# Performance work log

Measured on AMD Instinct MI355X. Metric: run time of the kernel, lower is better.

The kernel has to match this reference:

```python
import jax, jax.numpy as jnp
import numpy as np

DIM = 768
NUM_HEADS = 12
HEAD_DIM = DIM // NUM_HEADS
HIDDEN = int(DIM * 4.0)
EPS = 1e-8


def layer_norm(x, w, b):
    mu = jnp.mean(x, axis=-1, keepdims=True)
    var = jnp.mean(jnp.square(x - mu), axis=-1, keepdims=True)
    return (x - mu) * jax.lax.rsqrt(var + EPS) * w + b


def setup_inputs() -> dict:
    key = jax.random.key(0)
    ks = jax.random.split(key, 10)
    s = 0.02
    return {
        "x": jax.random.normal(ks[0], (16, 4096, DIM), dtype=jnp.float32),
        # Linear weights stored as [in, out]
        "qkv_w": jax.random.normal(ks[1], (DIM, 3 * DIM), dtype=jnp.float32) * s,
        "qkv_b": jnp.zeros((3 * DIM,), dtype=jnp.float32),
        "proj_w": jax.random.normal(ks[2], (DIM, DIM), dtype=jnp.float32) * s,
        "proj_b": jnp.zeros((DIM,), dtype=jnp.float32),
        "fc1_w": jax.random.normal(ks[3], (DIM, HIDDEN), dtype=jnp.float32) * s,
        "fc1_b": jnp.zeros((HIDDEN,), dtype=jnp.float32),
        "fc2_w": jax.random.normal(ks[4], (HIDDEN, DIM), dtype=jnp.float32) * s,
        "fc2_b": jnp.zeros((DIM,), dtype=jnp.float32),
        "ln1_w": jnp.ones((DIM,), dtype=jnp.float32),
        "ln1_b": jnp.zeros((DIM,), dtype=jnp.float32),
        "ln2_w": jnp.ones((DIM,), dtype=jnp.float32),
        "ln2_b": jnp.zeros((DIM,), dtype=jnp.float32),
    }


def linear_attention(x, qkv_w, qkv_b, proj_w, proj_b):
    B, N, C = x.shape
    qkv = (x @ qkv_w + qkv_b).reshape(B, N, 3, NUM_HEADS, HEAD_DIM)
    qkv = qkv.transpose(2, 0, 3, 1, 4)  # [3, B, H, N, D]
    q, k, v = qkv[0], qkv[1], qkv[2]
    q = jax.nn.elu(q) + 1.0
    k = jax.nn.elu(k) + 1.0
    kv = jnp.einsum('bhsd,bhse->bhde', k, v)          # [B,H,D,D]
    z = 1.0 / jnp.einsum('bhsd,bhd->bhs', q, k.sum(axis=-2))  # [B,H,N]
    out = jnp.einsum('bhde,bhsd,bhs->bhse', kv, q, z)  # [B,H,N,D]
    out = out.transpose(0, 2, 1, 3).reshape(B, N, C)
    return out @ proj_w + proj_b


def reference(x, qkv_w, qkv_b, proj_w, proj_b, fc1_w, fc1_b, fc2_w, fc2_b,
              ln1_w, ln1_b, ln2_w, ln2_b):
    y = linear_attention(layer_norm(x, ln1_w, ln1_b), qkv_w, qkv_b, proj_w, proj_b)
    x = x + y
    h = layer_norm(x, ln2_w, ln2_b)
    h = jax.nn.gelu(h @ fc1_w + fc1_b, approximate=False) @ fc2_w + fc2_b
    return x + h
```

## Files before the change

### kernel.cpp

```cpp
#include <hip/hip_runtime.h>

#define DEVI __device__ __forceinline__

typedef __attribute__((ext_vector_type(8))) short bf16x8;
typedef __attribute__((ext_vector_type(4))) float f32x4;
typedef __attribute__((ext_vector_type(4))) unsigned short usx4;

DEVI float bf2f(unsigned short u) {
  unsigned int b = ((unsigned int)u) << 16;
  float f;
  __builtin_memcpy(&f, &b, 4);
  return f;
}
DEVI unsigned short f2bf(float f) {
  unsigned int x;
  __builtin_memcpy(&x, &f, 4);
  x += 0x7FFFu + ((x >> 16) & 1u);
  return (unsigned short)(x >> 16);
}
DEVI void gload_lds16(const void* g, void* l) {
  __builtin_amdgcn_global_load_lds((const __attribute__((address_space(1))) void*)g,
                                   (__attribute__((address_space(3))) void*)l,
                                   16, 0, 0);
}

__global__ __launch_bounds__(256) void wt_kernel(const float* __restrict__ W,
                                                 unsigned short* __restrict__ Wt,
                                                 int K, int N) {
  __shared__ float t[32][33];
  const int tx = threadIdx.x & 31, ty = threadIdx.x >> 5;
  const int n0 = blockIdx.x * 32, k0 = blockIdx.y * 32;
#pragma unroll
  for (int i = 0; i < 4; ++i)
    t[ty * 4 + i][tx] = W[(size_t)(k0 + ty * 4 + i) * N + n0 + tx];
  __syncthreads();
#pragma unroll
  for (int i = 0; i < 4; ++i)
    Wt[(size_t)(n0 + ty * 4 + i) * K + k0 + tx] = f2bf(t[tx][ty * 4 + i]);
}

__global__ __launch_bounds__(256) void ln_kernel(const float* __restrict__ x,
                                                 const float* __restrict__ w,
                                                 const float* __restrict__ b,
                                                 unsigned short* __restrict__ o) {
  const int lane = threadIdx.x & 63;
  const int wave = threadIdx.x >> 6;
  const size_t row = (size_t)blockIdx.x * 4 + wave;
  const float* xr = x + row * 768;
  float v[12];
  float s = 0.f, sq = 0.f;
#pragma unroll
  for (int i = 0; i < 3; ++i) {
    const float4 f = *(const float4*)&xr[i * 256 + lane * 4];
    v[i * 4 + 0] = f.x; v[i * 4 + 1] = f.y; v[i * 4 + 2] = f.z; v[i * 4 + 3] = f.w;
    s += f.x + f.y + f.z + f.w;
    sq += f.x * f.x + f.y * f.y + f.z * f.z + f.w * f.w;
  }
#pragma unroll
  for (int off = 32; off > 0; off >>= 1) {
    s += __shfl_xor(s, off);
    sq += __shfl_xor(sq, off);
  }
  const float mu = s * (1.f / 768.f);
  const float rs = rsqrtf(sq * (1.f / 768.f) - mu * mu + 1e-8f);
  unsigned short* orow = o + row * 768;
#pragma unroll
  for (int i = 0; i < 3; ++i) {
    usx4 st;
#pragma unroll
    for (int j = 0; j < 4; ++j) {
      const int c = i * 256 + lane * 4 + j;
      st[j] = f2bf((v[i * 4 + j] - mu) * rs * w[c] + b[c]);
    }
    *(usx4*)&orow[i * 256 + lane * 4] = st;
  }
}

__global__ __launch_bounds__(256) void fuse_kernel(const float* __restrict__ x,
                                                   const unsigned short* __restrict__ y,
                                                   const float* __restrict__ w,
                                                   const float* __restrict__ b,
                                                   float* __restrict__ x2,
                                                   unsigned short* __restrict__ o) {
  const int lane = threadIdx.x & 63;
  const int wave = threadIdx.x >> 6;
  const size_t row = (size_t)blockIdx.x * 4 + wave;
  const float* xr = x + row * 768;
  const unsigned short* yr = y + row * 768;
  float* x2r = x2 + row * 768;
  float v[12];
  float s = 0.f, sq = 0.f;
#pragma unroll
  for (int i = 0; i < 3; ++i) {
    const float4 f = *(const float4*)&xr[i * 256 + lane * 4];
    const usx4 yv = *(const usx4*)&yr[i * 256 + lane * 4];
    float t0 = f.x + bf2f(yv[0]);
    float t1 = f.y + bf2f(yv[1]);
    float t2 = f.z + bf2f(yv[2]);
    float t3 = f.w + bf2f(yv[3]);
    v[i * 4 + 0] = t0; v[i * 4 + 1] = t1; v[i * 4 + 2] = t2; v[i * 4 + 3] = t3;
    s += t0 + t1 + t2 + t3;
    sq += t0 * t0 + t1 * t1 + t2 * t2 + t3 * t3;
    float4 fo; fo.x = t0; fo.y = t1; fo.z = t2; fo.w = t3;
    *(float4*)&x2r[i * 256 + lane * 4] = fo;
  }
#pragma unroll
  for (int off = 32; off > 0; off >>= 1) {
    s += __shfl_xor(s, off);
    sq += __shfl_xor(sq, off);
  }
  const float mu = s * (1.f / 768.f);
  const float rs = rsqrtf(sq * (1.f / 768.f) - mu * mu + 1e-8f);
  unsigned short* orow = o + row * 768;
#pragma unroll
  for (int i = 0; i < 3; ++i) {
    usx4 st;
#pragma unroll
    for (int j = 0; j < 4; ++j) {
      const int c = i * 256 + lane * 4 + j;
      st[j] = f2bf((v[i * 4 + j] - mu) * rs * w[c] + b[c]);
    }
    *(usx4*)&orow[i * 256 + lane * 4] = st;
  }
}

template <int EPI>
__global__ __launch_bounds__(512, 2) void gemm256_k(
    const unsigned short* __restrict__ A, const unsigned short* __restrict__ Bt,
    const float* __restrict__ bias, int N, int K,
    unsigned short* __restrict__ O0, unsigned short* __restrict__ O1,
    unsigned short* __restrict__ O2, float* __restrict__ OF) {
  __shared__ char lds[131072];
  const int tid = threadIdx.x;
  const int lane = tid & 63, wave = tid >> 6;
  const int wr = wave >> 2, wc = wave & 3;

  const int gx = gridDim.x;
  const int nwg = gx * gridDim.y;
  const int cpx = nwg >> 3;
  const int wgid = blockIdx.x + gx * blockIdx.y;
  const int v = (wgid & 7) * cpx + (wgid >> 3);
  const size_t n0 = (size_t)(v % gx) * 256;
  const size_t m0 = (size_t)(v / gx) * 256;

  const size_t ldg = (size_t)K * 2;
  const char* Abase = (const char*)A + m0 * ldg;
  const char* Bbase = (const char*)Bt + n0 * ldg;

  const int q0 = tid, q1 = tid + 512;
  const int rp0 = q0 >> 3, rp1 = q1 >> 3;
  const int lc0 = (q0 & 7) ^ (rp0 & 7), lc1 = (q1 & 7) ^ (rp1 & 7);
  const size_t go0 = (size_t)(rp0 * 2 + (lc0 >> 2)) * ldg + (size_t)(lc0 & 3) * 16;
  const size_t go1 = (size_t)(rp1 * 2 + (lc1 >> 2)) * ldg + (size_t)(lc1 & 3) * 16;
  const char* aS0 = Abase + go0;
  const char* aS1 = Abase + go1;
  const char* bS0 = Bbase + go0;
  const char* bS1 = Bbase + go1;
  char* ldsb = (char*)lds;
  const int d0 = tid * 16, d1 = 8192 + tid * 16;

  f32x4 acc[8][4];
#pragma unroll
  for (int m = 0; m < 8; ++m)
#pragma unroll
    for (int n = 0; n < 4; ++n) acc[m][n] = f32x4{0.f, 0.f, 0.f, 0.f};

  const int L = lane & 15, kc4 = lane >> 4;
  const int pcv = (((L & 1) << 2) | kc4) ^ (L >> 1);
  const int aro = wr * 8192 + (L >> 1) * 128 + pcv * 16;
  const int bro = 16384 + wc * 4096 + (L >> 1) * 128 + pcv * 16;

  const int nt = K >> 5;

#define STAGE(tt)                                              \
  do {                                                         \
    char* dst_ = ldsb + ((tt) & 3) * 32768;                    \
    const size_t ko_ = (size_t)(tt) * 64;                      \
    gload_lds16(aS0 + ko_, dst_ + d0);                         \
    gload_lds16(aS1 + ko_, dst_ + d1);                         \
    gload_lds16(bS0 + ko_, dst_ + 16384 + d0);                 \
    gload_lds16(bS1 + ko_, dst_ + 16384 + d1);                 \
  } while (0)

  STAGE(0);
  STAGE(1);
  STAGE(2);

  for (int t = 0; t < nt; ++t) {
    const int rem = nt - t;
    if (rem > 2)
      asm volatile("s_waitcnt vmcnt(8) lgkmcnt(0)" ::: "memory");
    else if (rem == 2)
      asm volatile("s_waitcnt vmcnt(4) lgkmcnt(0)" ::: "memory");
    else
      asm volatile("s_waitcnt vmcnt(0) lgkmcnt(0)" ::: "memory");
    __builtin_amdgcn_s_barrier();
    asm volatile("" ::: "memory");
    if (t + 3 < nt) STAGE(t + 3);
    const char* base = ldsb + (t & 3) * 32768;
    bf16x8 bF[4];
#pragma unroll
    for (int n = 0; n < 4; ++n) bF[n] = *(const bf16x8*)(base + bro + n * 1024);
    {
      bf16x8 aF[4];
#pragma unroll
      for (int m = 0; m < 4; ++m) aF[m] = *(const bf16x8*)(base + aro + m * 1024);
      __builtin_amdgcn_s_setprio(1);
#pragma unroll
      for (int m = 0; m < 4; ++m)
#pragma unroll
        for (int n = 0; n < 4; ++n)
          acc[m][n] = __builtin_amdgcn_mfma_f32_16x16x32_bf16(aF[m], bF[n], acc[m][n], 0, 0, 0);
      __builtin_amdgcn_s_setprio(0);
    }
    {
      bf16x8 aF[4];
#pragma unroll
      for (int m = 0; m < 4; ++m) aF[m] = *(const bf16x8*)(base + aro + (m + 4) * 1024);
      __builtin_amdgcn_s_setprio(1);
#pragma unroll
      for (int m = 0; m < 4; ++m)
#pragma unroll
        for (int n = 0; n < 4; ++n)
          acc[m + 4][n] = __builtin_amdgcn_mfma_f32_16x16x32_bf16(aF[m], bF[n], acc[m + 4][n], 0, 0, 0);
      __builtin_amdgcn_s_setprio(0);
    }
  }
#undef STAGE

  const int rl = (lane >> 4) * 4;
  const int cl = lane & 15;
#pragma unroll
  for (int m = 0; m < 8; ++m) {
    const size_t r0 = m0 + wr * 128 + m * 16 + rl;
#pragma unroll
    for (int n = 0; n < 4; ++n) {
      const size_t c = n0 + wc * 64 + n * 16 + cl;
      const float bv = bias[c];
      if (EPI == 0) {
#pragma unroll
        for (int j = 0; j < 4; ++j) O0[(r0 + j) * (size_t)N + c] = f2bf(acc[m][n][j] + bv);
      } else if (EPI == 1) {
#pragma unroll
        for (int j = 0; j < 4; ++j) {
          float val = acc[m][n][j] + bv;
          val = 0.5f * val * (1.0f + erff(val * 0.70710678118654752f));
          O0[(r0 + j) * (size_t)N + c] = f2bf(val);
        }
      } else if (EPI == 2) {
        const int t = (int)(c / 768);
        const int rem = (int)c - t * 768;
        const int h = rem >> 6, d = rem & 63;
        const int b = (int)(r0 >> 12);
        const int s = (int)(r0 & 4095);
        const size_t bh = (size_t)b * 12 + h;
        if (t == 0) {
#pragma unroll
          for (int j = 0; j < 4; ++j) {
            float val = acc[m][n][j] + bv;
            val = val > 0.f ? val + 1.f : __expf(val);
            O0[(bh * 4096 + (size_t)(s + j)) * 64 + d] = f2bf(val);
          }
        } else {
          usx4 st;
#pragma unroll
          for (int j = 0; j < 4; ++j) {
            float val = acc[m][n][j] + bv;
            if (t == 1) val = val > 0.f ? val + 1.f : __expf(val);
            st[j] = f2bf(val);
          }
          unsigned short* dst = (t == 1) ? O1 : O2;
          *(usx4*)&dst[(bh * 64 + d) * 4096 + s] = st;
        }
      } else {
#pragma unroll
        for (int j = 0; j < 4; ++j) {
          const size_t idx = (r0 + j) * (size_t)N + c;
          OF[idx] += acc[m][n][j] + bv;
        }
      }
    }
  }
}

__global__ __launch_bounds__(256) void kv_kernel(const unsigned short* __restrict__ kT,
                                                 const unsigned short* __restrict__ vT,
                                                 float* __restrict__ kvT) {
  __shared__ float red[4 * 64 * 64];
  const int tid = threadIdx.x;
  const int lane = tid & 63, wave = tid >> 6;
  const size_t bh = blockIdx.x;
  const unsigned short* kb = kT + bh * (size_t)(64 * 4096);
  const unsigned short* vb = vT + bh * (size_t)(64 * 4096);
  f32x4 acc[4][4];
#pragma unroll
  for (int m = 0; m < 4; ++m)
#pragma unroll
    for (int n = 0; n < 4; ++n) acc[m][n] = f32x4{0.f, 0.f, 0.f, 0.f};
  const int kh = (lane >> 4) * 8;
  for (int st = 0; st < 32; ++st) {
    const int s0 = wave * 1024 + st * 32 + kh;
    bf16x8 aF[4], bF[4];
#pragma unroll
    for (int m = 0; m < 4; ++m)
      aF[m] = *(const bf16x8*)&kb[(size_t)((lane & 15) + 16 * m) * 4096 + s0];
#pragma unroll
    for (int n = 0; n < 4; ++n)
      bF[n] = *(const bf16x8*)&vb[(size_t)((lane & 15) + 16 * n) * 4096 + s0];
#pragma unroll
    for (int m = 0; m < 4; ++m)
#pragma unroll
      for (int n = 0; n < 4; ++n)
        acc[m][n] = __builtin_amdgcn_mfma_f32_16x16x32_bf16(aF[m], bF[n], acc[m][n], 0, 0, 0);
  }
#pragma unroll
  for (int m = 0; m < 4; ++m)
#pragma unroll
    for (int n = 0; n < 4; ++n)
#pragma unroll
      for (int j = 0; j < 4; ++j)
        red[wave * 4096 + (m * 16 + (lane >> 4) * 4 + j) * 64 + n * 16 + (lane & 15)] =
            acc[m][n][j];
  __syncthreads();
  for (int i = 0; i < 16; ++i) {
    const int f = i * 256 + tid;
    float s = 0.f;
#pragma unroll
    for (int w = 0; w < 4; ++w) s += red[w * 4096 + f];
    const int d = f >> 6, e = f & 63;
    kvT[bh * 4096 + e * 64 + d] = s;
  }
}

__global__ __launch_bounds__(256) void ksum_kernel(const unsigned short* __restrict__ kT,
                                                   float* __restrict__ ksum) {
  __shared__ float part[256];
  const int tid = threadIdx.x;
  const int d = tid & 63, p = tid >> 6;
  const size_t bh = blockIdx.x;
  const unsigned short* kb = kT + bh * (size_t)(64 * 4096) + (size_t)d * 4096 + p * 1024;
  float s = 0.f;
  for (int i = 0; i < 128; ++i) {
    const bf16x8 v = *(const bf16x8*)&kb[i * 8];
#pragma unroll
    for (int j = 0; j < 8; ++j) s += bf2f((unsigned short)v[j]);
  }
  part[tid] = s;
  __syncthreads();
  if (tid < 64) ksum[bh * 64 + d] = part[d] + part[64 + d] + part[128 + d] + part[192 + d];
}

__global__ __launch_bounds__(256) void attn_out_kernel(const unsigned short* __restrict__ q,
                                                       const float* __restrict__ kvT,
                                                       const float* __restrict__ ksum,
                                                       unsigned short* __restrict__ attnout) {
  __shared__ float kvl[4096];
  __shared__ float ksl[64];
  __shared__ float zl[4 * 64];
  const int tid = threadIdx.x;
  const int lane = tid & 63, wave = tid >> 6;
  const int bh = blockIdx.x >> 2;
  const int chunk = blockIdx.x & 3;
  const int b = bh / 12, h = bh % 12;
  const float* kvb = kvT + (size_t)bh * 4096;
  for (int i = tid; i < 4096; i += 256) kvl[i] = kvb[i];
  if (tid < 64) ksl[tid] = ksum[(size_t)bh * 64 + tid];
  __syncthreads();

  const int kh = (lane >> 4) * 8;
  bf16x8 bF[4], ksF;
#pragma unroll
  for (int n = 0; n < 4; ++n) {
    bf16x8 t;
#pragma unroll
    for (int j = 0; j < 8; ++j)
      t[j] = (short)f2bf(kvl[((lane & 15) + 16 * n) * 64 + kh + j]);
    bF[n] = t;
  }
  {
    bf16x8 t;
#pragma unroll
    for (int j = 0; j < 8; ++j)
      t[j] = ((lane & 15) == 0) ? (short)f2bf(ksl[kh + j]) : (short)0;
    ksF = t;
  }
  const unsigned short* qb = q + (size_t)bh * 4096 * 64;

  for (int st = 0; st < 4; ++st) {
    const int s0 = chunk * 1024 + wave * 256 + st * 64;
    bf16x8 aF[4];
#pragma unroll
    for (int m = 0; m < 4; ++m)
      aF[m] = *(const bf16x8*)&qb[(size_t)(s0 + (lane & 15) + 16 * m) * 64 + kh];
    f32x4 acc[4][4];
    f32x4 dacc[4];
#pragma unroll
    for (int m = 0; m < 4; ++m) {
      dacc[m] = f32x4{0.f, 0.f, 0.f, 0.f};
#pragma unroll
      for (int n = 0; n < 4; ++n) acc[m][n] = f32x4{0.f, 0.f, 0.f, 0.f};
    }
#pragma unroll
    for (int m = 0; m < 4; ++m) {
#pragma unroll
      for (int n = 0; n < 4; ++n)
        acc[m][n] = __builtin_amdgcn_mfma_f32_16x16x32_bf16(aF[m], bF[n], acc[m][n], 0, 0, 0);
      dacc[m] = __builtin_amdgcn_mfma_f32_16x16x32_bf16(aF[m], ksF, dacc[m], 0, 0, 0);
    }
    if ((lane & 15) == 0) {
#pragma unroll
      for (int m = 0; m < 4; ++m)
#pragma unroll
        for (int j = 0; j < 4; ++j)
          zl[wave * 64 + m * 16 + (lane >> 4) * 4 + j] = 1.0f / dacc[m][j];
    }
    __syncthreads();
#pragma unroll
    for (int m = 0; m < 4; ++m)
#pragma unroll
      for (int n = 0; n < 4; ++n)
#pragma unroll
        for (int j = 0; j < 4; ++j) {
          const int sl = m * 16 + (lane >> 4) * 4 + j;
          const int s = s0 + sl;
          const float val = acc[m][n][j] * zl[wave * 64 + sl];
          const int e = n * 16 + (lane & 15);
          attnout[((size_t)b * 4096 + s) * 768 + h * 64 + e] = f2bf(val);
        }
    __syncthreads();
  }
}

extern "C" void kernel_launch(void* const* d_in, const int* in_sizes, int n_in,
                              void* d_out, int out_size, void* d_ws, size_t ws_size,
                              hipStream_t stream) {
  const float* x = (const float*)d_in[0];
  const float* qkv_w = (const float*)d_in[1];
  const float* qkv_b = (const float*)d_in[2];
  const float* proj_w = (const float*)d_in[3];
  const float* proj_b = (const float*)d_in[4];
  const float* fc1_w = (const float*)d_in[5];
  const float* fc1_b = (const float*)d_in[6];
  const float* fc2_w = (const float*)d_in[7];
  const float* fc2_b = (const float*)d_in[8];
  const float* ln1_w = (const float*)d_in[9];
  const float* ln1_b = (const float*)d_in[10];
  const float* ln2_w = (const float*)d_in[11];
  const float* ln2_b = (const float*)d_in[12];
  float* out = (float*)d_out;

  char* ws = (char*)d_ws;
  const size_t PL = (size_t)65536 * 768 * 2;
  unsigned short* xn = (unsigned short*)(ws + 0 * PL);
  unsigned short* q = (unsigned short*)(ws + 1 * PL);
  unsigned short* kT = (unsigned short*)(ws + 2 * PL);
  unsigned short* vT = (unsigned short*)(ws + 3 * PL);
  unsigned short* attnout = xn;
  unsigned short* ybuf = kT;
  unsigned short* xn2 = (unsigned short*)(ws + 4 * PL);
  unsigned short* hbuf = (unsigned short*)(ws + 0 * PL);
  size_t off = 5 * PL;
  float* kvT = (float*)(ws + off); off += (size_t)192 * 4096 * 4;
  float* ksum = (float*)(ws + off); off += (size_t)192 * 64 * 4;
  unsigned short* qkvWt = (unsigned short*)(ws + off); off += (size_t)2304 * 768 * 2;
  unsigned short* projWt = (unsigned short*)(ws + off); off += (size_t)768 * 768 * 2;
  unsigned short* fc1Wt = (unsigned short*)(ws + off); off += (size_t)3072 * 768 * 2;
  unsigned short* fc2Wt = (unsigned short*)(ws + off); off += (size_t)768 * 3072 * 2;

  wt_kernel<<<dim3(72, 24), 256, 0, stream>>>(qkv_w, qkvWt, 768, 2304);
  wt_kernel<<<dim3(24, 24), 256, 0, stream>>>(proj_w, projWt, 768, 768);
  wt_kernel<<<dim3(96, 24), 256, 0, stream>>>(fc1_w, fc1Wt, 768, 3072);
  wt_kernel<<<dim3(24, 96), 256, 0, stream>>>(fc2_w, fc2Wt, 3072, 768);
  ln_kernel<<<16384, 256, 0, stream>>>(x, ln1_w, ln1_b, xn);
  gemm256_k<2><<<dim3(9, 256), 512, 0, stream>>>(xn, qkvWt, qkv_b, 2304, 768, q, kT, vT, nullptr);
  ksum_kernel<<<192, 256, 0, stream>>>(kT, ksum);
  kv_kernel<<<192, 256, 0, stream>>>(kT, vT, kvT);
  attn_out_kernel<<<768, 256, 0, stream>>>(q, kvT, ksum, attnout);
  gemm256_k<0><<<dim3(3, 256), 512, 0, stream>>>(attnout, projWt, proj_b, 768, 768, ybuf, nullptr,
                                                 nullptr, nullptr);
  fuse_kernel<<<16384, 256, 0, stream>>>(x, ybuf, ln2_w, ln2_b, out, xn2);
  gemm256_k<1><<<dim3(12, 256), 512, 0, stream>>>(xn2, fc1Wt, fc1_b, 3072, 768, hbuf, nullptr,
                                                  nullptr, nullptr);
  gemm256_k<3><<<dim3(3, 256), 512, 0, stream>>>(hbuf, fc2Wt, fc2_b, 768, 3072, nullptr, nullptr,
                                                 nullptr, out);
  (void)in_sizes; (void)n_in; (void)out_size; (void)ws_size;
}
```

Baseline: 1.734 ms.

## Split GEMM prefetch into A/B halves interleaved with MFMA and stage QKV transpose via LDS

The GEMM main loop now issues the A-tile prefetch and the B-tile prefetch separately, each placed between the two MFMA half-blocks with barriers and sched_barriers. This interleaves global-to-LDS traffic and LDS fragment reads with matrix math instead of issuing all loads at the top of the iteration. The QKV epilogue for the K and V transposed outputs is also rewritten to stage the tile in swizzled LDS per wave and then write contiguous rows along the sequence dimension. The wait-count logic is reworked to match, which risks subtle ordering errors and adds an extra barrier per iteration.

```diff
diff --git a/kernel.cpp b/kernel.cpp
--- a/kernel.cpp
+++ b/kernel.cpp
@@ -165,71 +165,136 @@
 #pragma unroll
     for (int n = 0; n < 4; ++n) acc[m][n] = f32x4{0.f, 0.f, 0.f, 0.f};
 
-  const int L = lane & 15, kc4 = lane >> 4;
+  const int L = lane & 15;
+  const int kc4 = lane >> 4;
   const int pcv = (((L & 1) << 2) | kc4) ^ (L >> 1);
   const int aro = wr * 8192 + (L >> 1) * 128 + pcv * 16;
   const int bro = 16384 + wc * 4096 + (L >> 1) * 128 + pcv * 16;
 
   const int nt = K >> 5;
 
-#define STAGE(tt)                                              \
+#define STAGE_A(tt)                                            \
   do {                                                         \
     char* dst_ = ldsb + ((tt) & 3) * 32768;                    \
     const size_t ko_ = (size_t)(tt) * 64;                      \
     gload_lds16(aS0 + ko_, dst_ + d0);                         \
     gload_lds16(aS1 + ko_, dst_ + d1);                         \
+  } while (0)
+#define STAGE_B(tt)                                            \
+  do {                                                         \
+    char* dst_ = ldsb + ((tt) & 3) * 32768;                    \
+    const size_t ko_ = (size_t)(tt) * 64;                      \
     gload_lds16(bS0 + ko_, dst_ + 16384 + d0);                 \
     gload_lds16(bS1 + ko_, dst_ + 16384 + d1);                 \
   } while (0)
 
-  STAGE(0);
-  STAGE(1);
-  STAGE(2);
+  STAGE_A(0); STAGE_B(0);
+  STAGE_A(1); STAGE_B(1);
+  STAGE_A(2); STAGE_B(2);
+  asm volatile("s_waitcnt vmcnt(8)" ::: "memory");
+  __builtin_amdgcn_s_barrier();
 
   for (int t = 0; t < nt; ++t) {
-    const int rem = nt - t;
-    if (rem > 2)
-      asm volatile("s_waitcnt vmcnt(8) lgkmcnt(0)" ::: "memory");
-    else if (rem == 2)
-      asm volatile("s_waitcnt vmcnt(4) lgkmcnt(0)" ::: "memory");
-    else
-      asm volatile("s_waitcnt vmcnt(0) lgkmcnt(0)" ::: "memory");
+    const char* base = ldsb + (t & 3) * 32768;
+    bf16x8 bF[4], aF0[4];
+#pragma unroll
+    for (int n = 0; n < 4; ++n) bF[n] = *(const bf16x8*)(base + bro + n * 1024);
+#pragma unroll
+    for (int m = 0; m < 4; ++m) aF0[m] = *(const bf16x8*)(base + aro + m * 1024);
+    if (t + 3 < nt) STAGE_A(t + 3);
+    asm volatile("s_waitcnt lgkmcnt(0)" ::: "memory");
     __builtin_amdgcn_s_barrier();
-    asm volatile("" ::: "memory");
-    if (t + 3 < nt) STAGE(t + 3);
-    const char* base = ldsb + (t & 3) * 32768;
-    bf16x8 bF[4];
-#pragma unroll
-    for (int n = 0; n < 4; ++n) bF[n] = *(const bf16x8*)(base + bro + n * 1024);
+    __builtin_amdgcn_sched_barrier(0);
+    __builtin_amdgcn_s_setprio(1);
+#pragma unroll
+    for (int m = 0; m < 4; ++m)
+#pragma unroll
+      for (int n = 0; n < 4; ++n)
+        acc[m][n] = __builtin_amdgcn_mfma_f32_16x16x32_bf16(aF0[m], bF[n], acc[m][n], 0, 0, 0);
+    __builtin_amdgcn_s_setprio(0);
+    __builtin_amdgcn_sched_barrier(0);
+    bf16x8 aF1[4];
+#pragma unroll
+    for (int m = 0; m < 4; ++m) aF1[m] = *(const bf16x8*)(base + aro + (m + 4) * 1024);
+    if (t + 3 < nt) STAGE_B(t + 3);
     {
-      bf16x8 aF[4];
-#pragma unroll
-      for (int m = 0; m < 4; ++m) aF[m] = *(const bf16x8*)(base + aro + m * 1024);
-      __builtin_amdgcn_s_setprio(1);
-#pragma unroll
-      for (int m = 0; m < 4; ++m)
-#pragma unroll
-        for (int n = 0; n < 4; ++n)
-          acc[m][n] = __builtin_amdgcn_mfma_f32_16x16x32_bf16(aF[m], bF[n], acc[m][n], 0, 0, 0);
-      __builtin_amdgcn_s_setprio(0);
-    }
-    {
-      bf16x8 aF[4];
-#pragma unroll
-      for (int m = 0; m < 4; ++m) aF[m] = *(const bf16x8*)(base + aro + (m + 4) * 1024);
-      __builtin_amdgcn_s_setprio(1);
-#pragma unroll
-      for (int m = 0; m < 4; ++m)
-#pragma unroll
-        for (int n = 0; n < 4; ++n)
-          acc[m + 4][n] = __builtin_amdgcn_mfma_f32_16x16x32_bf16(aF[m], bF[n], acc[m + 4][n], 0, 0, 0);
-      __builtin_amdgcn_s_setprio(0);
-    }
-  }
-#undef STAGE
+      const int rem = nt - t;
+      if (rem >= 4)
+        asm volatile("s_waitcnt vmcnt(8) lgkmcnt(0)" ::: "memory");
+      else if (rem == 3)
+        asm volatile("s_waitcnt vmcnt(4) lgkmcnt(0)" ::: "memory");
+      else
+        asm volatile("s_waitcnt vmcnt(0) lgkmcnt(0)" ::: "memory");
+    }
+    __builtin_amdgcn_s_barrier();
+    __builtin_amdgcn_sched_barrier(0);
+    __builtin_amdgcn_s_setprio(1);
+#pragma unroll
+    for (int m = 0; m < 4; ++m)
+#pragma unroll
+      for (int n = 0; n < 4; ++n)
+        acc[m + 4][n] = __builtin_amdgcn_mfma_f32_16x16x32_bf16(aF1[m], bF[n], acc[m + 4][n], 0, 0, 0);
+    __builtin_amdgcn_s_setprio(0);
+    __builtin_amdgcn_sched_barrier(0);
+  }
+#undef STAGE_A
+#undef STAGE_B
 
   const int rl = (lane >> 4) * 4;
   const int cl = lane & 15;
+
+  if (EPI == 2) {
+    const int cbase = (int)n0 + wc * 64;
+    const int tsec = cbase / 768;
+    const int h = (cbase - tsec * 768) >> 6;
+    const int rbase = (int)m0 + wr * 128;
+    const int b = rbase >> 12;
+    const int s0w = rbase & 4095;
+    const size_t bh = (size_t)b * 12 + h;
+    if (tsec == 0) {
+#pragma unroll
+      for (int m = 0; m < 8; ++m)
+#pragma unroll
+        for (int n = 0; n < 4; ++n) {
+          const int d = n * 16 + cl;
+          const float bv = bias[cbase + d];
+#pragma unroll
+          for (int j = 0; j < 4; ++j) {
+            float val = acc[m][n][j] + bv;
+            val = val > 0.f ? val + 1.f : __expf(val);
+            O0[(bh * 4096 + (size_t)(s0w + m * 16 + rl + j)) * 64 + d] = f2bf(val);
+          }
+        }
+    } else {
+      unsigned short* dst = (tsec == 1) ? O1 : O2;
+      char* wlds = ldsb + wave * 16384;
+#pragma unroll
+      for (int m = 0; m < 8; ++m)
+#pragma unroll
+        for (int n = 0; n < 4; ++n) {
+          const int c2 = n * 16 + cl;
+          const float bv = bias[cbase + c2];
+          usx4 st;
+#pragma unroll
+          for (int j = 0; j < 4; ++j) {
+            float val = acc[m][n][j] + bv;
+            if (tsec == 1) val = val > 0.f ? val + 1.f : __expf(val);
+            st[j] = f2bf(val);
+          }
+          const int r2 = m * 16 + rl;
+          *(usx4*)(wlds + c2 * 256 + ((r2 * 2) ^ ((c2 & 7) << 5))) = st;
+        }
+      asm volatile("s_waitcnt lgkmcnt(0)" ::: "memory");
+#pragma unroll 4
+      for (int dl = 0; dl < 64; ++dl) {
+        const unsigned int pr =
+            *(const unsigned int*)(wlds + dl * 256 + ((lane * 4) ^ ((dl & 7) << 5)));
+        *(unsigned int*)&dst[(bh * 64 + dl) * 4096 + (size_t)(s0w + lane * 2)] = pr;
+      }
+    }
+    return;
+  }
+
 #pragma unroll
   for (int m = 0; m < 8; ++m) {
     const size_t r0 = m0 + wr * 128 + m * 16 + rl;
@@ -246,31 +311,6 @@
           float val = acc[m][n][j] + bv;
           val = 0.5f * val * (1.0f + erff(val * 0.70710678118654752f));
           O0[(r0 + j) * (size_t)N + c] = f2bf(val);
-        }
-      } else if (EPI == 2) {
-        const int t = (int)(c / 768);
-        const int rem = (int)c - t * 768;
-        const int h = rem >> 6, d = rem & 63;
-        const int b = (int)(r0 >> 12);
-        const int s = (int)(r0 & 4095);
-        const size_t bh = (size_t)b * 12 + h;
-        if (t == 0) {
-#pragma unroll
-          for (int j = 0; j < 4; ++j) {
-            float val = acc[m][n][j] + bv;
-            val = val > 0.f ? val + 1.f : __expf(val);
-            O0[(bh * 4096 + (size_t)(s + j)) * 64 + d] = f2bf(val);
-          }
-        } else {
-          usx4 st;
-#pragma unroll
-          for (int j = 0; j < 4; ++j) {
-            float val = acc[m][n][j] + bv;
-            if (t == 1) val = val > 0.f ? val + 1.f : __expf(val);
-            st[j] = f2bf(val);
-          }
-          unsigned short* dst = (t == 1) ? O1 : O2;
-          *(usx4*)&dst[(bh * 64 + d) * 4096 + s] = st;
         }
       } else {
 #pragma unroll
```

New measurement: 1.637 ms. 5.6% less time.

## Shrink GEMM tiles to 128x256 with double buffering and fuse ksum into kv kernel

Applied to the files above, without the earlier changes.

The GEMM moves from a 256x256 tile with a 4-stage, 128KB LDS pipeline to a 128x256 tile with a 2-stage, 48KB LDS pipeline, aiming for higher occupancy and more workgroups. The QKV epilogue now writes K and V row-major ([bh, s, d]) instead of transposed, with per-wave head decoding. The kv kernel is rewritten to stage K and V chunks through swizzled LDS and to compute the k-sum in the same pass, dropping the separate ksum launch. The tradeoffs are lower per-tile data reuse, an extra barrier per K-step, and scalar strided epilogue stores.

```diff
diff --git a/kernel.cpp b/kernel.cpp
--- a/kernel.cpp
+++ b/kernel.cpp
@@ -125,12 +125,12 @@
 }
 
 template <int EPI>
-__global__ __launch_bounds__(512, 2) void gemm256_k(
+__global__ __launch_bounds__(512, 4) void gemm_k(
     const unsigned short* __restrict__ A, const unsigned short* __restrict__ Bt,
     const float* __restrict__ bias, int N, int K,
     unsigned short* __restrict__ O0, unsigned short* __restrict__ O1,
     unsigned short* __restrict__ O2, float* __restrict__ OF) {
-  __shared__ char lds[131072];
+  __shared__ unsigned short sm[24576];
   const int tid = threadIdx.x;
   const int lane = tid & 63, wave = tid >> 6;
   const int wr = wave >> 2, wc = wave & 3;
@@ -141,98 +141,99 @@
   const int wgid = blockIdx.x + gx * blockIdx.y;
   const int v = (wgid & 7) * cpx + (wgid >> 3);
   const size_t n0 = (size_t)(v % gx) * 256;
-  const size_t m0 = (size_t)(v / gx) * 256;
-
-  const size_t ldg = (size_t)K * 2;
-  const char* Abase = (const char*)A + m0 * ldg;
-  const char* Bbase = (const char*)Bt + n0 * ldg;
-
-  const int q0 = tid, q1 = tid + 512;
-  const int rp0 = q0 >> 3, rp1 = q1 >> 3;
-  const int lc0 = (q0 & 7) ^ (rp0 & 7), lc1 = (q1 & 7) ^ (rp1 & 7);
-  const size_t go0 = (size_t)(rp0 * 2 + (lc0 >> 2)) * ldg + (size_t)(lc0 & 3) * 16;
-  const size_t go1 = (size_t)(rp1 * 2 + (lc1 >> 2)) * ldg + (size_t)(lc1 & 3) * 16;
-  const char* aS0 = Abase + go0;
-  const char* aS1 = Abase + go1;
-  const char* bS0 = Bbase + go0;
-  const char* bS1 = Bbase + go1;
-  char* ldsb = (char*)lds;
-  const int d0 = tid * 16, d1 = 8192 + tid * 16;
-
-  f32x4 acc[8][4];
-#pragma unroll
-  for (int m = 0; m < 8; ++m)
+  const size_t m0 = (size_t)(v / gx) * 128;
+
+  const int rA = tid >> 2;
+  const int cA = (tid & 3) ^ ((rA ^ (rA >> 2)) & 3);
+  const unsigned short* srcA = A + (m0 + rA) * (size_t)K + cA * 8;
+  const unsigned short* srcB0 = Bt + (n0 + rA) * (size_t)K + cA * 8;
+  const unsigned short* srcB1 = srcB0 + (size_t)128 * K;
+
+  unsigned short* smA = sm;
+  unsigned short* smB = sm + 8192;
+
+  f32x4 acc[4][4];
+#pragma unroll
+  for (int m = 0; m < 4; ++m)
 #pragma unroll
     for (int n = 0; n < 4; ++n) acc[m][n] = f32x4{0.f, 0.f, 0.f, 0.f};
 
   const int L = lane & 15, kc4 = lane >> 4;
-  const int pcv = (((L & 1) << 2) | kc4) ^ (L >> 1);
-  const int aro = wr * 8192 + (L >> 1) * 128 + pcv * 16;
-  const int bro = 16384 + wc * 4096 + (L >> 1) * 128 + pcv * 16;
+  const int fL = (L ^ (L >> 2)) & 3;
+  const int aoff = (wr * 64 + L) * 32 + ((kc4 ^ fL) << 3);
+  const int boff = (wc * 64 + L) * 32 + ((kc4 ^ fL) << 3);
 
   const int nt = K >> 5;
 
 #define STAGE(tt)                                              \
   do {                                                         \
-    char* dst_ = ldsb + ((tt) & 3) * 32768;                    \
-    const size_t ko_ = (size_t)(tt) * 64;                      \
-    gload_lds16(aS0 + ko_, dst_ + d0);                         \
-    gload_lds16(aS1 + ko_, dst_ + d1);                         \
-    gload_lds16(bS0 + ko_, dst_ + 16384 + d0);                 \
-    gload_lds16(bS1 + ko_, dst_ + 16384 + d1);                 \
+    const int p_ = (tt) & 1;                                   \
+    const size_t ko_ = (size_t)(tt) * 32;                      \
+    gload_lds16(srcA + ko_, smA + p_ * 4096 + tid * 8);        \
+    gload_lds16(srcB0 + ko_, smB + p_ * 8192 + tid * 8);       \
+    gload_lds16(srcB1 + ko_, smB + p_ * 8192 + 4096 + tid * 8);\
   } while (0)
 
   STAGE(0);
   STAGE(1);
-  STAGE(2);
 
   for (int t = 0; t < nt; ++t) {
-    const int rem = nt - t;
-    if (rem > 2)
-      asm volatile("s_waitcnt vmcnt(8) lgkmcnt(0)" ::: "memory");
-    else if (rem == 2)
-      asm volatile("s_waitcnt vmcnt(4) lgkmcnt(0)" ::: "memory");
+    if (t + 1 < nt)
+      asm volatile("s_waitcnt vmcnt(3)" ::: "memory");
     else
-      asm volatile("s_waitcnt vmcnt(0) lgkmcnt(0)" ::: "memory");
+      asm volatile("s_waitcnt vmcnt(0)" ::: "memory");
     __builtin_amdgcn_s_barrier();
-    asm volatile("" ::: "memory");
-    if (t + 3 < nt) STAGE(t + 3);
-    const char* base = ldsb + (t & 3) * 32768;
-    bf16x8 bF[4];
-#pragma unroll
-    for (int n = 0; n < 4; ++n) bF[n] = *(const bf16x8*)(base + bro + n * 1024);
-    {
-      bf16x8 aF[4];
-#pragma unroll
-      for (int m = 0; m < 4; ++m) aF[m] = *(const bf16x8*)(base + aro + m * 1024);
-      __builtin_amdgcn_s_setprio(1);
-#pragma unroll
-      for (int m = 0; m < 4; ++m)
-#pragma unroll
-        for (int n = 0; n < 4; ++n)
-          acc[m][n] = __builtin_amdgcn_mfma_f32_16x16x32_bf16(aF[m], bF[n], acc[m][n], 0, 0, 0);
-      __builtin_amdgcn_s_setprio(0);
-    }
-    {
-      bf16x8 aF[4];
-#pragma unroll
-      for (int m = 0; m < 4; ++m) aF[m] = *(const bf16x8*)(base + aro + (m + 4) * 1024);
-      __builtin_amdgcn_s_setprio(1);
-#pragma unroll
-      for (int m = 0; m < 4; ++m)
-#pragma unroll
-        for (int n = 0; n < 4; ++n)
-          acc[m + 4][n] = __builtin_amdgcn_mfma_f32_16x16x32_bf16(aF[m], bF[n], acc[m + 4][n], 0, 0, 0);
-      __builtin_amdgcn_s_setprio(0);
-    }
+    const unsigned short* Abase = smA + (t & 1) * 4096 + aoff;
+    const unsigned short* Bbase = smB + (t & 1) * 8192 + boff;
+    bf16x8 aF[4], bF[4];
+#pragma unroll
+    for (int m = 0; m < 4; ++m) aF[m] = *(const bf16x8*)(Abase + m * 512);
+#pragma unroll
+    for (int n = 0; n < 4; ++n) bF[n] = *(const bf16x8*)(Bbase + n * 512);
+    asm volatile("s_waitcnt lgkmcnt(0)" ::: "memory");
+    __builtin_amdgcn_s_barrier();
+    if (t + 2 < nt) STAGE(t + 2);
+    __builtin_amdgcn_s_setprio(1);
+#pragma unroll
+    for (int m = 0; m < 4; ++m)
+#pragma unroll
+      for (int n = 0; n < 4; ++n)
+        acc[m][n] = __builtin_amdgcn_mfma_f32_16x16x32_bf16(aF[m], bF[n], acc[m][n], 0, 0, 0);
+    __builtin_amdgcn_s_setprio(0);
   }
 #undef STAGE
 
   const int rl = (lane >> 4) * 4;
   const int cl = lane & 15;
-#pragma unroll
-  for (int m = 0; m < 8; ++m) {
-    const size_t r0 = m0 + wr * 128 + m * 16 + rl;
+
+  if (EPI == 2) {
+    const int cbase = (int)n0 + wc * 64;
+    const int tsec = cbase / 768;
+    const int h = (cbase - tsec * 768) >> 6;
+    const int rbase = (int)m0 + wr * 64;
+    const int b = rbase >> 12;
+    const int s0w = rbase & 4095;
+    const size_t bh = (size_t)b * 12 + h;
+    unsigned short* dst = (tsec == 0) ? O0 : (tsec == 1 ? O1 : O2);
+#pragma unroll
+    for (int m = 0; m < 4; ++m)
+#pragma unroll
+      for (int n = 0; n < 4; ++n) {
+        const int d = n * 16 + cl;
+        const float bv = bias[cbase + d];
+#pragma unroll
+        for (int j = 0; j < 4; ++j) {
+          float val = acc[m][n][j] + bv;
+          if (tsec < 2) val = val > 0.f ? val + 1.f : __expf(val);
+          dst[(bh * 4096 + (size_t)(s0w + m * 16 + rl + j)) * 64 + d] = f2bf(val);
+        }
+      }
+    return;
+  }
+
+#pragma unroll
+  for (int m = 0; m < 4; ++m) {
+    const size_t r0 = m0 + wr * 64 + m * 16 + rl;
 #pragma unroll
     for (int n = 0; n < 4; ++n) {
       const size_t c = n0 + wc * 64 + n * 16 + cl;
@@ -247,31 +248,6 @@
           val = 0.5f * val * (1.0f + erff(val * 0.70710678118654752f));
           O0[(r0 + j) * (size_t)N + c] = f2bf(val);
         }
-      } else if (EPI == 2) {
-        const int t = (int)(c / 768);
-        const int rem = (int)c - t * 768;
-        const int h = rem >> 6, d = rem & 63;
-        const int b = (int)(r0 >> 12);
-        const int s = (int)(r0 & 4095);
-        const size_t bh = (size_t)b * 12 + h;
-        if (t == 0) {
-#pragma unroll
-          for (int j = 0; j < 4; ++j) {
-            float val = acc[m][n][j] + bv;
-            val = val > 0.f ? val + 1.f : __expf(val);
-            O0[(bh * 4096 + (size_t)(s + j)) * 64 + d] = f2bf(val);
-          }
-        } else {
-          usx4 st;
-#pragma unroll
-          for (int j = 0; j < 4; ++j) {
-            float val = acc[m][n][j] + bv;
-            if (t == 1) val = val > 0.f ? val + 1.f : __expf(val);
-            st[j] = f2bf(val);
-          }
-          unsigned short* dst = (t == 1) ? O1 : O2;
-          *(usx4*)&dst[(bh * 64 + d) * 4096 + s] = st;
-        }
       } else {
 #pragma unroll
         for (int j = 0; j < 4; ++j) {
@@ -283,71 +259,90 @@
   }
 }
 
-__global__ __launch_bounds__(256) void kv_kernel(const unsigned short* __restrict__ kT,
-                                                 const unsigned short* __restrict__ vT,
-                                                 float* __restrict__ kvT) {
-  __shared__ float red[4 * 64 * 64];
-  const int tid = threadIdx.x;
-  const int lane = tid & 63, wave = tid >> 6;
+__global__ __launch_bounds__(256) void kv_kernel(const unsigned short* __restrict__ k,
+                                                 const unsigned short* __restrict__ v,
+                                                 float* __restrict__ kvT,
+                                                 float* __restrict__ ksum) {
+  __shared__ unsigned short kl[8192];
+  __shared__ unsigned short vl[8192];
+  __shared__ float red[256];
+  const int tid = threadIdx.x, lane = tid & 63, wave = tid >> 6;
   const size_t bh = blockIdx.x;
-  const unsigned short* kb = kT + bh * (size_t)(64 * 4096);
-  const unsigned short* vb = vT + bh * (size_t)(64 * 4096);
-  f32x4 acc[4][4];
-#pragma unroll
-  for (int m = 0; m < 4; ++m)
-#pragma unroll
-    for (int n = 0; n < 4; ++n) acc[m][n] = f32x4{0.f, 0.f, 0.f, 0.f};
-  const int kh = (lane >> 4) * 8;
+  const unsigned short* kb = k + bh * (size_t)(4096 * 64);
+  const unsigned short* vb = v + bh * (size_t)(4096 * 64);
+  f32x4 acc[4];
+#pragma unroll
+  for (int n = 0; n < 4; ++n) acc[n] = f32x4{0.f, 0.f, 0.f, 0.f};
+  float ks = 0.f;
+
+  const int r = tid >> 1;
+  const int hf = tid & 1;
+  const int c4 = r >> 5;
+  const int scw = (r >> 3) & 3;
+  int wofs[4];
+#pragma unroll
+  for (int dd = 0; dd < 4; ++dd)
+    wofs[dd] = c4 * 32 + ((scw ^ ((c4 ^ dd) & 3)) << 3) + (r & 7);
+
+  const int L = lane & 15, kc4 = lane >> 4;
+  const int dA = wave * 16 + L;
+  const int dq = tid & 63, q4 = tid >> 6;
+  const int Fks = (q4 ^ dq) & 3;
+  const int ksbase = (dq * 4 + q4) * 32;
+
   for (int st = 0; st < 32; ++st) {
-    const int s0 = wave * 1024 + st * 32 + kh;
-    bf16x8 aF[4], bF[4];
-#pragma unroll
-    for (int m = 0; m < 4; ++m)
-      aF[m] = *(const bf16x8*)&kb[(size_t)((lane & 15) + 16 * m) * 4096 + s0];
-#pragma unroll
-    for (int n = 0; n < 4; ++n)
-      bF[n] = *(const bf16x8*)&vb[(size_t)((lane & 15) + 16 * n) * 4096 + s0];
-#pragma unroll
-    for (int m = 0; m < 4; ++m)
-#pragma unroll
-      for (int n = 0; n < 4; ++n)
-        acc[m][n] = __builtin_amdgcn_mfma_f32_16x16x32_bf16(aF[m], bF[n], acc[m][n], 0, 0, 0);
-  }
-#pragma unroll
-  for (int m = 0; m < 4; ++m)
-#pragma unroll
-    for (int n = 0; n < 4; ++n)
-#pragma unroll
-      for (int j = 0; j < 4; ++j)
-        red[wave * 4096 + (m * 16 + (lane >> 4) * 4 + j) * 64 + n * 16 + (lane & 15)] =
-            acc[m][n][j];
+    const int s0 = st * 128;
+    __syncthreads();
+    {
+      const unsigned short* krow = kb + (size_t)(s0 + r) * 64 + hf * 32;
+      const unsigned short* vrow = vb + (size_t)(s0 + r) * 64 + hf * 32;
+      bf16x8 kk[4], vv[4];
+#pragma unroll
+      for (int g = 0; g < 4; ++g) {
+        kk[g] = *(const bf16x8*)(krow + g * 8);
+        vv[g] = *(const bf16x8*)(vrow + g * 8);
+      }
+#pragma unroll
+      for (int g = 0; g < 4; ++g)
+#pragma unroll
+        for (int i = 0; i < 8; ++i) {
+          const int d = hf * 32 + g * 8 + i;
+          const int a = d * 128 + wofs[d & 3];
+          kl[a] = (unsigned short)kk[g][i];
+          vl[a] = (unsigned short)vv[g][i];
+        }
+    }
+    __syncthreads();
+#pragma unroll
+    for (int scc = 0; scc < 4; ++scc) {
+      const bf16x8 t8 = *(const bf16x8*)&kl[ksbase + ((scc ^ Fks) << 3)];
+#pragma unroll
+      for (int i = 0; i < 8; ++i) ks += bf2f((unsigned short)t8[i]);
+    }
+#pragma unroll
+    for (int ksl = 0; ksl < 4; ++ksl) {
+      const int physA = kc4 ^ ((ksl ^ dA) & 3);
+      const bf16x8 aF = *(const bf16x8*)&kl[(dA * 4 + ksl) * 32 + physA * 8];
+#pragma unroll
+      for (int n = 0; n < 4; ++n) {
+        const int e = n * 16 + L;
+        const int physB = kc4 ^ ((ksl ^ e) & 3);
+        const bf16x8 bF = *(const bf16x8*)&vl[(e * 4 + ksl) * 32 + physB * 8];
+        acc[n] = __builtin_amdgcn_mfma_f32_16x16x32_bf16(aF, bF, acc[n], 0, 0, 0);
+      }
+    }
+  }
+  red[tid] = ks;
   __syncthreads();
-  for (int i = 0; i < 16; ++i) {
-    const int f = i * 256 + tid;
-    float s = 0.f;
-#pragma unroll
-    for (int w = 0; w < 4; ++w) s += red[w * 4096 + f];
-    const int d = f >> 6, e = f & 63;
-    kvT[bh * 4096 + e * 64 + d] = s;
-  }
-}
-
-__global__ __launch_bounds__(256) void ksum_kernel(const unsigned short* __restrict__ kT,
-                                                   float* __restrict__ ksum) {
-  __shared__ float part[256];
-  const int tid = threadIdx.x;
-  const int d = tid & 63, p = tid >> 6;
-  const size_t bh = blockIdx.x;
-  const unsigned short* kb = kT + bh * (size_t)(64 * 4096) + (size_t)d * 4096 + p * 1024;
-  float s = 0.f;
-  for (int i = 0; i < 128; ++i) {
-    const bf16x8 v = *(const bf16x8*)&kb[i * 8];
-#pragma unroll
-    for (int j = 0; j < 8; ++j) s += bf2f((unsigned short)v[j]);
-  }
-  part[tid] = s;
-  __syncthreads();
-  if (tid < 64) ksum[bh * 64 + d] = part[d] + part[64 + d] + part[128 + d] + part[192 + d];
+  if (tid < 64) ksum[bh * 64 + tid] = red[tid] + red[64 + tid] + red[128 + tid] + red[192 + tid];
+#pragma unroll
+  for (int n = 0; n < 4; ++n)
+#pragma unroll
+    for (int j = 0; j < 4; ++j) {
+      const int d = wave * 16 + (lane >> 4) * 4 + j;
+      const int e = n * 16 + (lane & 15);
+      kvT[bh * 4096 + e * 64 + d] = acc[n][j];
+    }
 }
 
 __global__ __launch_bounds__(256) void attn_out_kernel(const unsigned short* __restrict__ q,
@@ -453,10 +448,10 @@
   const size_t PL = (size_t)65536 * 768 * 2;
   unsigned short* xn = (unsigned short*)(ws + 0 * PL);
   unsigned short* q = (unsigned short*)(ws + 1 * PL);
-  unsigned short* kT = (unsigned short*)(ws + 2 * PL);
-  unsigned short* vT = (unsigned short*)(ws + 3 * PL);
+  unsigned short* kbuf = (unsigned short*)(ws + 2 * PL);
+  unsigned short* vbuf = (unsigned short*)(ws + 3 * PL);
   unsigned short* attnout = xn;
-  unsigned short* ybuf = kT;
+  unsigned short* ybuf = kbuf;
   unsigned short* xn2 = (unsigned short*)(ws + 4 * PL);
   unsigned short* hbuf = (unsigned short*)(ws + 0 * PL);
   size_t off = 5 * PL;
@@ -472,16 +467,15 @@
   wt_kernel<<<dim3(96, 24), 256, 0, stream>>>(fc1_w, fc1Wt, 768, 3072);
   wt_kernel<<<dim3(24, 96), 256, 0, stream>>>(fc2_w, fc2Wt, 3072, 768);
   ln_kernel<<<16384, 256, 0, stream>>>(x, ln1_w, ln1_b, xn);
-  gemm256_k<2><<<dim3(9, 256), 512, 0, stream>>>(xn, qkvWt, qkv_b, 2304, 768, q, kT, vT, nullptr);
-  ksum_kernel<<<192, 256, 0, stream>>>(kT, ksum);
-  kv_kernel<<<192, 256, 0, stream>>>(kT, vT, kvT);
+  gemm_k<2><<<dim3(9, 512), 512, 0, stream>>>(xn, qkvWt, qkv_b, 2304, 768, q, kbuf, vbuf, nullptr);
+  kv_kernel<<<192, 256, 0, stream>>>(kbuf, vbuf, kvT, ksum);
   attn_out_kernel<<<768, 256, 0, stream>>>(q, kvT, ksum, attnout);
-  gemm256_k<0><<<dim3(3, 256), 512, 0, stream>>>(attnout, projWt, proj_b, 768, 768, ybuf, nullptr,
-                                                 nullptr, nullptr);
+  gemm_k<0><<<dim3(3, 512), 512, 0, stream>>>(attnout, projWt, proj_b, 768, 768, ybuf, nullptr,
+                                              nullptr, nullptr);
   fuse_kernel<<<16384, 256, 0, stream>>>(x, ybuf, ln2_w, ln2_b, out, xn2);
-  gemm256_k<1><<<dim3(12, 256), 512, 0, stream>>>(xn2, fc1Wt, fc1_b, 3072, 768, hbuf, nullptr,
-                                                  nullptr, nullptr);
-  gemm256_k<3><<<dim3(3, 256), 512, 0, stream>>>(hbuf, fc2Wt, fc2_b, 768, 3072, nullptr, nullptr,
-                                                 nullptr, out);
+  gemm_k<1><<<dim3(12, 512), 512, 0, stream>>>(xn2, fc1Wt, fc1_b, 3072, 768, hbuf, nullptr,
+                                               nullptr, nullptr);
+  gemm_k<3><<<dim3(3, 512), 512, 0, stream>>>(hbuf, fc2Wt, fc2_b, 768, 3072, nullptr, nullptr,
+                                              nullptr, out);
   (void)in_sizes; (void)n_in; (void)out_size; (void)ws_size;
 }
```

After: 1.547 ms. -10.8%, faster.
